# Optimization experiments

Measured on AMD Instinct MI355X. Metric: run time of the kernel, lower is better.

The kernel has to match this reference:

```python
import jax, jax.numpy as jnp
import numpy as np

WS = 7          # window size
NH = 16         # n_heads
DIM = 512
HEAD_DIM = DIM // NH
SCALE = HEAD_DIM ** -0.5


def _rel_pos_index(ws):
    coords = np.stack(np.meshgrid(np.arange(ws), np.arange(ws), indexing='ij'))  # [2,ws,ws]
    coords = coords.reshape(2, -1)                                               # [2,N]
    rel = coords[:, :, None] - coords[:, None, :]                                # [2,N,N]
    idx = (rel[0] + ws - 1) * (2 * ws - 1) + (rel[1] + ws - 1)                   # [N,N]
    return jnp.asarray(idx, dtype=jnp.int32)


def _window_partition(x, ws):
    B, H, W, C = x.shape
    x = x.reshape(B, H // ws, ws, W // ws, ws, C)
    x = x.transpose(0, 1, 3, 2, 4, 5)
    return x.reshape(-1, ws * ws, C)  # [B*nW, N, C]


def setup_inputs() -> dict:
    key = jax.random.key(0)
    k1, k2, k3 = jax.random.split(key, 3)
    qkv = jax.random.normal(k1, (3, 32, 56, 56, DIM), dtype=jnp.float32)
    mask = jax.random.normal(k2, (64, WS * WS, WS * WS), dtype=jnp.float32)
    bias_table = jax.random.normal(k3, ((2 * WS - 1) ** 2, NH), dtype=jnp.float32) * 0.02
    return {"qkv": qkv, "mask": mask, "bias_table": bias_table}


def reference(qkv, mask, bias_table):
    q, k, v = qkv[0], qkv[1], qkv[2]
    B, H, W, C = q.shape
    N = WS * WS
    # window partition + split heads -> [BS, NH, N, HEAD_DIM]
    def prep(x):
        x = _window_partition(x, WS)                       # [BS, N, C]
        BS = x.shape[0]
        return x.reshape(BS, N, NH, HEAD_DIM).transpose(0, 2, 1, 3)
    q, k, v = prep(q), prep(k), prep(v)
    BS = q.shape[0]

    attn = jnp.einsum('bhnd,bhmd->bhnm', q, k) * SCALE      # [BS, NH, N, N]

    idx = _rel_pos_index(WS)                                # [N, N] static
    rel_bias = bias_table[idx]                              # [N, N, NH]
    attn = attn + rel_bias.transpose(2, 0, 1)[None]         # [BS, NH, N, N]

    nW = mask.shape[0]
    attn = attn.reshape(BS // nW, nW, NH, N, N) + mask[None, :, None]
    attn = attn.reshape(BS, NH, N, N)

    attn = jax.nn.softmax(attn, axis=-1)
    x = jnp.einsum('bhnm,bhmd->bhnd', attn, v)              # [BS, NH, N, HEAD_DIM]
    return x.transpose(0, 2, 1, 3).reshape(BS, N, C)
```

## Files before the change

### kernel.cpp

```cpp
#include <hip/hip_runtime.h>

#define NTOK 49
#define NH 16
#define DIM 512
#define HD 32
#define HPB 4
#define SCALE 0.17677669529663687f
#define NEGINF -3.0e38f

typedef __attribute__((ext_vector_type(8))) short short8;
typedef __attribute__((ext_vector_type(16))) float f32x16;

struct __attribute__((packed, aligned(4))) f4u { float x, y, z, w; };

__device__ __forceinline__ unsigned short fb(float x) {
    return __builtin_bit_cast(unsigned short, (__bf16)x);
}

__device__ __forceinline__ float b2f(unsigned short b) {
    union { unsigned u; float f; } v; v.u = ((unsigned)b) << 16;
    return v.f;
}

__device__ __forceinline__ unsigned long long pk4(float4 v) {
    unsigned lo = (unsigned)fb(v.x) | ((unsigned)fb(v.y) << 16);
    unsigned hi = (unsigned)fb(v.z) | ((unsigned)fb(v.w) << 16);
    return (unsigned long long)lo | ((unsigned long long)hi << 32);
}

__device__ __forceinline__ short8 pk8s(float4 a, float4 b, float sc) {
    short8 r;
    r[0] = (short)fb(a.x * sc); r[1] = (short)fb(a.y * sc);
    r[2] = (short)fb(a.z * sc); r[3] = (short)fb(a.w * sc);
    r[4] = (short)fb(b.x * sc); r[5] = (short)fb(b.y * sc);
    r[6] = (short)fb(b.z * sc); r[7] = (short)fb(b.w * sc);
    return r;
}

__global__ __launch_bounds__(256, 4) void winattn_mfma(
    const float* __restrict__ qkv,
    const float* __restrict__ mask,
    const float* __restrict__ bias_table,
    float* __restrict__ out)
{
    __shared__ __align__(16) unsigned short Vr[HPB][64][32];
    __shared__ __align__(8)  unsigned short maskw[HPB][2404];
    __shared__ float biasw[HPB][176];
    __shared__ float invl[HPB][64];

    const int bx   = blockIdx.x;
    const int win  = bx >> 2;
    const int hg   = bx & 3;
    const int tid  = threadIdx.x;
    const int wave = tid >> 6;
    const int lane = tid & 63;
    const int ln   = lane & 31;
    const int h    = lane >> 5;
    const int head = hg * HPB + wave;

    const int b  = win >> 6;
    const int w  = win & 63;
    const int wr = w >> 3, wc = w & 7;

    const size_t plane = (size_t)32 * 56 * 56 * 512;
    const size_t wbase = (((size_t)(b * 56 + wr * 7)) * 56 + wc * 7) * 512 + head * HD;

    const int t0 = ln;
    const int t1 = (32 + ln <= 48) ? (32 + ln) : 48;
    float4 qv[2][4], kv[2][4];
    #pragma unroll
    for (int tt = 0; tt < 2; ++tt) {
        const int t  = tt ? t1 : t0;
        const int i  = t / 7, j = t - i * 7;
        const float* qp = qkv + wbase + (size_t)(i * 56 + j) * 512 + h * 8;
        const float* kp = qp + plane;
        qv[tt][0] = *(const float4*)(qp);
        qv[tt][1] = *(const float4*)(qp + 4);
        qv[tt][2] = *(const float4*)(qp + 16);
        qv[tt][3] = *(const float4*)(qp + 20);
        kv[tt][0] = *(const float4*)(kp);
        kv[tt][1] = *(const float4*)(kp + 4);
        kv[tt][2] = *(const float4*)(kp + 16);
        kv[tt][3] = *(const float4*)(kp + 20);
    }

    #pragma unroll
    for (int e = 0; e < 8; ++e) {
        const int idx = e * 64 + lane;
        const int t   = idx >> 3;
        const int d4  = idx & 7;
        unsigned long long vz = 0;
        if (t < NTOK) {
            const int i = t / 7, j = t - i * 7;
            vz = pk4(*(const float4*)(qkv + 2 * plane + wbase
                                      + (size_t)(i * 56 + j) * 512 + d4 * 4));
        }
        *(unsigned long long*)&Vr[wave][t][d4 * 4] = vz;
    }

    const float* mrow = mask + (size_t)w * 2401;
    for (int e = lane; e < 600; e += 64) {
        f4u mv = *(const f4u*)(mrow + 4 * e);
        unsigned long long pk =
              (unsigned long long)fb(mv.x)
            | ((unsigned long long)fb(mv.y) << 16)
            | ((unsigned long long)fb(mv.z) << 32)
            | ((unsigned long long)fb(mv.w) << 48);
        *(unsigned long long*)&maskw[wave][4 * e] = pk;
    }
    if (lane == 0) maskw[wave][2400] = fb(mrow[2400]);

    for (int r = lane; r < 169; r += 64)
        biasw[wave][r] = bias_table[r * NH + head];

    short8 qfr[2][2], kfr[2][2];
    #pragma unroll
    for (int tt = 0; tt < 2; ++tt) {
        qfr[tt][0] = pk8s(qv[tt][0], qv[tt][1], SCALE);
        qfr[tt][1] = pk8s(qv[tt][2], qv[tt][3], SCALE);
        kfr[tt][0] = pk8s(kv[tt][0], kv[tt][1], 1.0f);
        kfr[tt][1] = pk8s(kv[tt][2], kv[tt][3], 1.0f);
    }

    f32x16 zer;
    #pragma unroll
    for (int i = 0; i < 16; ++i) zer[i] = 0.f;
    f32x16 acc[2][2];
    acc[0][0] = zer; acc[0][1] = zer; acc[1][0] = zer; acc[1][1] = zer;
    #pragma unroll
    for (int ks = 0; ks < 2; ++ks) {
        acc[0][0] = __builtin_amdgcn_mfma_f32_32x32x16_bf16(kfr[0][ks], qfr[0][ks], acc[0][0], 0, 0, 0);
        acc[0][1] = __builtin_amdgcn_mfma_f32_32x32x16_bf16(kfr[0][ks], qfr[1][ks], acc[0][1], 0, 0, 0);
        acc[1][0] = __builtin_amdgcn_mfma_f32_32x32x16_bf16(kfr[1][ks], qfr[0][ks], acc[1][0], 0, 0, 0);
        acc[1][1] = __builtin_amdgcn_mfma_f32_32x32x16_bf16(kfr[1][ks], qfr[1][ks], acc[1][1], 0, 0, 0);
    }

    unsigned wpk[2][2][8];
    #pragma unroll
    for (int nt = 0; nt < 2; ++nt) {
        const int n  = 32 * nt + ln;
        const int nc = n < NTOK ? n : NTOK - 1;
        const int i_n = nc / 7;
        const int tn  = nc + 6 * i_n + 84;
        float sum = 0.f;
        #pragma unroll
        for (int mt = 0; mt < 2; ++mt) {
            #pragma unroll
            for (int g = 0; g < 8; ++g) {
                const int ia = (g < 4) ? g : g + 4;
                float e0, e1;
                {
                    const int mb  = 32 * mt + (ia & 3) + 8 * (ia >> 2);
                    const int m0  = mb, m1 = mb + 4;
                    const int mc0 = m0 < NTOK ? m0 : NTOK - 1;
                    const int mc1 = m1 < NTOK ? m1 : NTOK - 1;
                    const int tm0 = mc0 + 6 * (mc0 / 7);
                    const int tm1 = mc1 + 6 * (mc1 / 7);
                    const int mc  = h ? mc1 : mc0;
                    const int tm  = h ? tm1 : tm0;
                    float s = acc[mt][nt][ia] + biasw[wave][tn - tm]
                            + b2f(maskw[wave][nc * NTOK + mc]);
                    const bool dead = h ? (m1 >= NTOK) : (m0 >= NTOK);
                    e0 = __expf(dead ? NEGINF : s);
                }
                {
                    const int rb  = ia + 4;
                    const int mb  = 32 * mt + (rb & 3) + 8 * (rb >> 2);
                    const int m0  = mb, m1 = mb + 4;
                    if (m0 >= NTOK && m1 >= NTOK) {
                        e1 = 0.f;
                    } else {
                        const int mc0 = m0 < NTOK ? m0 : NTOK - 1;
                        const int mc1 = m1 < NTOK ? m1 : NTOK - 1;
                        const int tm0 = mc0 + 6 * (mc0 / 7);
                        const int tm1 = mc1 + 6 * (mc1 / 7);
                        const int mc  = h ? mc1 : mc0;
                        const int tm  = h ? tm1 : tm0;
                        float s = acc[mt][nt][rb] + biasw[wave][tn - tm]
                                + b2f(maskw[wave][nc * NTOK + mc]);
                        const bool dead = h ? (m1 >= NTOK) : (m0 >= NTOK);
                        e1 = __expf(dead ? NEGINF : s);
                    }
                }
                sum += e0 + e1;
                wpk[nt][mt][g] = (unsigned)fb(e0) | ((unsigned)fb(e1) << 16);
            }
        }
        sum += __shfl_xor(sum, 32);
        if (h == 0 && n < NTOK)
            invl[wave][n] = 1.0f / sum;
    }

    f32x16 oacc[2];
    oacc[0] = zer; oacc[1] = zer;
    #pragma unroll
    for (int ksv = 0; ksv < 4; ++ksv) {
        short8 vf;
        #pragma unroll
        for (int j = 0; j < 8; ++j)
            vf[j] = (short)Vr[wave][16 * ksv + 8 * h + j][ln];
        const int mt = ksv >> 1;
        #pragma unroll
        for (int nt = 0; nt < 2; ++nt) {
            unsigned short alo[4], ahi[4];
            #pragma unroll
            for (int jj = 0; jj < 4; ++jj) {
                const unsigned W = wpk[nt][mt][(ksv & 1) * 4 + jj];
                const unsigned U = (unsigned)__shfl_xor((int)W, 32);
                alo[jj] = h ? (unsigned short)(U >> 16) : (unsigned short)(W & 0xffffu);
                ahi[jj] = h ? (unsigned short)(W >> 16) : (unsigned short)(U & 0xffffu);
            }
            short8 af;
            af[0] = (short)alo[0]; af[1] = (short)alo[1];
            af[2] = (short)alo[2]; af[3] = (short)alo[3];
            af[4] = (short)ahi[0]; af[5] = (short)ahi[1];
            af[6] = (short)ahi[2]; af[7] = (short)ahi[3];
            oacc[nt] = __builtin_amdgcn_mfma_f32_32x32x16_bf16(af, vf, oacc[nt], 0, 0, 0);
        }
    }

    const size_t obase = ((size_t)win * NTOK) * DIM + head * HD + ln;
    #pragma unroll
    for (int nt = 0; nt < 2; ++nt) {
        #pragma unroll
        for (int r = 0; r < 16; ++r) {
            const int nb = 32 * nt + (r & 3) + 8 * (r >> 2);
            const int n  = h ? nb + 4 : nb;
            if (n < NTOK)
                out[obase + (size_t)n * DIM] = oacc[nt][r] * invl[wave][n];
        }
    }
}

extern "C" void kernel_launch(void* const* d_in, const int* in_sizes, int n_in,
                              void* d_out, int out_size, void* d_ws, size_t ws_size,
                              hipStream_t stream) {
    const float* qkv        = (const float*)d_in[0];
    const float* mask       = (const float*)d_in[1];
    const float* bias_table = (const float*)d_in[2];
    float* out = (float*)d_out;

    winattn_mfma<<<2048 * 4, 256, 0, stream>>>(qkv, mask, bias_table, out);
}
```

Baseline: 188.2 us.

## Precompute combined mask+bias table in bf16 workspace via separate kernel

A new pre-pass kernel folds the window mask and the relative position bias into a single bf16 table per (window, head) in workspace. The main attention kernel then loads that precomputed table straight into shared memory and no longer gathers and adds mask and bias on the fly. The table is rebuilt on every call, so this is not cross-call reuse. It costs an extra launch and writes about 5 MB, and it rounds the bias to bf16. The old kernel remains as a fallback when the workspace is too small.

```diff
diff --git a/kernel.cpp b/kernel.cpp
--- a/kernel.cpp
+++ b/kernel.cpp
@@ -7,11 +7,10 @@
 #define HPB 4
 #define SCALE 0.17677669529663687f
 #define NEGINF -3.0e38f
+#define CSTR 2404
 
 typedef __attribute__((ext_vector_type(8))) short short8;
 typedef __attribute__((ext_vector_type(16))) float f32x16;
-
-struct __attribute__((packed, aligned(4))) f4u { float x, y, z, w; };
 
 __device__ __forceinline__ unsigned short fb(float x) {
     return __builtin_bit_cast(unsigned short, (__bf16)x);
@@ -37,7 +36,190 @@
     return r;
 }
 
-__global__ __launch_bounds__(256, 4) void winattn_mfma(
+__global__ __launch_bounds__(256) void comb_expand(
+    const float* __restrict__ mask, const float* __restrict__ bt,
+    unsigned short* __restrict__ comb)
+{
+    const int e = blockIdx.x * 256 + threadIdx.x;
+    if (e >= 64 * NH * CSTR) return;
+    const int r     = e % CSTR;
+    const int slice = e / CSTR;
+    const int head  = slice & 15;
+    const int w     = slice >> 4;
+    unsigned short v = 0;
+    if (r < NTOK * NTOK) {
+        const int n = r / NTOK, m = r % NTOK;
+        const int rel = (n / 7 - m / 7 + 6) * 13 + (n % 7 - m % 7 + 6);
+        v = fb(mask[(size_t)w * (NTOK * NTOK) + r] + bt[rel * NH + head]);
+    }
+    comb[e] = v;
+}
+
+__global__ __launch_bounds__(256, 4) void winattn_comb(
+    const float* __restrict__ qkv,
+    const unsigned short* __restrict__ comb,
+    float* __restrict__ out)
+{
+    __shared__ __align__(16) unsigned short Vr[HPB][64][32];
+    __shared__ __align__(8)  unsigned short combw[HPB][2460];
+    __shared__ float invl[HPB][64];
+
+    const int bx   = blockIdx.x;
+    const int win  = bx >> 2;
+    const int hg   = bx & 3;
+    const int tid  = threadIdx.x;
+    const int wave = tid >> 6;
+    const int lane = tid & 63;
+    const int ln   = lane & 31;
+    const int h    = lane >> 5;
+    const int head = hg * HPB + wave;
+
+    const int b  = win >> 6;
+    const int w  = win & 63;
+    const int wr = w >> 3, wc = w & 7;
+
+    const size_t plane = (size_t)32 * 56 * 56 * 512;
+    const size_t wbase = (((size_t)(b * 56 + wr * 7)) * 56 + wc * 7) * 512 + head * HD;
+
+    const int t0 = ln;
+    const int t1 = (32 + ln <= 48) ? (32 + ln) : 48;
+    float4 qv[2][4], kv[2][4];
+    #pragma unroll
+    for (int tt = 0; tt < 2; ++tt) {
+        const int t  = tt ? t1 : t0;
+        const int i  = t / 7, j = t - i * 7;
+        const float* qp = qkv + wbase + (size_t)(i * 56 + j) * 512 + h * 8;
+        const float* kp = qp + plane;
+        qv[tt][0] = *(const float4*)(qp);
+        qv[tt][1] = *(const float4*)(qp + 4);
+        qv[tt][2] = *(const float4*)(qp + 16);
+        qv[tt][3] = *(const float4*)(qp + 20);
+        kv[tt][0] = *(const float4*)(kp);
+        kv[tt][1] = *(const float4*)(kp + 4);
+        kv[tt][2] = *(const float4*)(kp + 16);
+        kv[tt][3] = *(const float4*)(kp + 20);
+    }
+
+    #pragma unroll
+    for (int e = 0; e < 8; ++e) {
+        const int idx = e * 64 + lane;
+        const int t   = idx >> 3;
+        const int d4  = idx & 7;
+        unsigned long long vz = 0;
+        if (t < NTOK) {
+            const int i = t / 7, j = t - i * 7;
+            vz = pk4(*(const float4*)(qkv + 2 * plane + wbase
+                                      + (size_t)(i * 56 + j) * 512 + d4 * 4));
+        }
+        *(unsigned long long*)&Vr[wave][t][d4 * 4] = vz;
+    }
+
+    const unsigned short* cg = comb + (size_t)((w << 4) | head) * CSTR;
+    for (int e = lane; e < CSTR / 4; e += 64)
+        *(unsigned long long*)&combw[wave][e * 4] = *(const unsigned long long*)(cg + e * 4);
+
+    short8 qfr[2][2], kfr[2][2];
+    #pragma unroll
+    for (int tt = 0; tt < 2; ++tt) {
+        qfr[tt][0] = pk8s(qv[tt][0], qv[tt][1], SCALE);
+        qfr[tt][1] = pk8s(qv[tt][2], qv[tt][3], SCALE);
+        kfr[tt][0] = pk8s(kv[tt][0], kv[tt][1], 1.0f);
+        kfr[tt][1] = pk8s(kv[tt][2], kv[tt][3], 1.0f);
+    }
+
+    f32x16 zer;
+    #pragma unroll
+    for (int i = 0; i < 16; ++i) zer[i] = 0.f;
+    f32x16 acc[2][2];
+    acc[0][0] = zer; acc[0][1] = zer; acc[1][0] = zer; acc[1][1] = zer;
+    #pragma unroll
+    for (int ks = 0; ks < 2; ++ks) {
+        acc[0][0] = __builtin_amdgcn_mfma_f32_32x32x16_bf16(kfr[0][ks], qfr[0][ks], acc[0][0], 0, 0, 0);
+        acc[0][1] = __builtin_amdgcn_mfma_f32_32x32x16_bf16(kfr[0][ks], qfr[1][ks], acc[0][1], 0, 0, 0);
+        acc[1][0] = __builtin_amdgcn_mfma_f32_32x32x16_bf16(kfr[1][ks], qfr[0][ks], acc[1][0], 0, 0, 0);
+        acc[1][1] = __builtin_amdgcn_mfma_f32_32x32x16_bf16(kfr[1][ks], qfr[1][ks], acc[1][1], 0, 0, 0);
+    }
+
+    unsigned wpk[2][2][8];
+    #pragma unroll
+    for (int nt = 0; nt < 2; ++nt) {
+        const int n  = 32 * nt + ln;
+        const int nc = n < NTOK ? n : NTOK - 1;
+        const unsigned short* crow = &combw[wave][nc * NTOK + 4 * h];
+        float sum = 0.f;
+        #pragma unroll
+        for (int g = 0; g < 8; ++g) {
+            const int ia = (g < 4) ? g : g + 4;
+            const int mb = (ia & 3) + 8 * (ia >> 2);
+            const float e0 = __expf(acc[0][nt][ia]     + b2f(crow[mb]));
+            const float e1 = __expf(acc[0][nt][ia + 4] + b2f(crow[mb + 8]));
+            sum += e0 + e1;
+            wpk[nt][0][g] = (unsigned)fb(e0) | ((unsigned)fb(e1) << 16);
+        }
+        #pragma unroll
+        for (int g = 0; g < 4; ++g) {
+            const int mb = 32 + g;
+            const float e0 = __expf(acc[1][nt][g]     + b2f(crow[mb]));
+            const float e1 = __expf(acc[1][nt][g + 4] + b2f(crow[mb + 8]));
+            sum += e0 + e1;
+            wpk[nt][1][g] = (unsigned)fb(e0) | ((unsigned)fb(e1) << 16);
+        }
+        {
+            const float s  = acc[1][nt][8] + b2f(crow[48]);
+            const float e0 = h ? 0.f : __expf(s);
+            sum += e0;
+            wpk[nt][1][4] = (unsigned)fb(e0);
+        }
+        wpk[nt][1][5] = 0u; wpk[nt][1][6] = 0u; wpk[nt][1][7] = 0u;
+        sum += __shfl_xor(sum, 32);
+        if (h == 0 && n < NTOK)
+            invl[wave][n] = 1.0f / sum;
+    }
+
+    f32x16 oacc[2];
+    oacc[0] = zer; oacc[1] = zer;
+    #pragma unroll
+    for (int ksv = 0; ksv < 4; ++ksv) {
+        short8 vf;
+        #pragma unroll
+        for (int j = 0; j < 8; ++j)
+            vf[j] = (short)Vr[wave][16 * ksv + 8 * h + j][ln];
+        const int mt = ksv >> 1;
+        #pragma unroll
+        for (int nt = 0; nt < 2; ++nt) {
+            unsigned short alo[4], ahi[4];
+            #pragma unroll
+            for (int jj = 0; jj < 4; ++jj) {
+                const unsigned W = wpk[nt][mt][(ksv & 1) * 4 + jj];
+                const unsigned U = (unsigned)__shfl_xor((int)W, 32);
+                alo[jj] = h ? (unsigned short)(U >> 16) : (unsigned short)(W & 0xffffu);
+                ahi[jj] = h ? (unsigned short)(W >> 16) : (unsigned short)(U & 0xffffu);
+            }
+            short8 af;
+            af[0] = (short)alo[0]; af[1] = (short)alo[1];
+            af[2] = (short)alo[2]; af[3] = (short)alo[3];
+            af[4] = (short)ahi[0]; af[5] = (short)ahi[1];
+            af[6] = (short)ahi[2]; af[7] = (short)ahi[3];
+            oacc[nt] = __builtin_amdgcn_mfma_f32_32x32x16_bf16(af, vf, oacc[nt], 0, 0, 0);
+        }
+    }
+
+    const size_t obase = ((size_t)win * NTOK) * DIM + head * HD + ln;
+    #pragma unroll
+    for (int nt = 0; nt < 2; ++nt) {
+        #pragma unroll
+        for (int r = 0; r < 16; ++r) {
+            const int nb = 32 * nt + (r & 3) + 8 * (r >> 2);
+            const int n  = h ? nb + 4 : nb;
+            if (n < NTOK)
+                out[obase + (size_t)n * DIM] = oacc[nt][r] * invl[wave][n];
+        }
+    }
+}
+
+struct __attribute__((packed, aligned(4))) f4u { float x, y, z, w; };
+
+__global__ __launch_bounds__(256, 4) void winattn_r9(
     const float* __restrict__ qkv,
     const float* __restrict__ mask,
     const float* __restrict__ bias_table,
@@ -240,5 +422,12 @@
     const float* bias_table = (const float*)d_in[2];
     float* out = (float*)d_out;
 
-    winattn_mfma<<<2048 * 4, 256, 0, stream>>>(qkv, mask, bias_table, out);
-}
+    const size_t comb_bytes = (size_t)64 * NH * CSTR * 2;
+    if (ws_size >= comb_bytes) {
+        unsigned short* comb = (unsigned short*)d_ws;
+        comb_expand<<<(64 * NH * CSTR + 255) / 256, 256, 0, stream>>>(mask, bias_table, comb);
+        winattn_comb<<<2048 * 4, 256, 0, stream>>>(qkv, comb, out);
+    } else {
+        winattn_r9<<<2048 * 4, 256, 0, stream>>>(qkv, mask, bias_table, out);
+    }
+}
```

Measured after the change: 207.4 us. +10.2%, slower.
